# Optimization experiments

Hardware: AMD Instinct MI355X
Metric: run time of the kernel (lower is better)

Reference implementation:

```python
import jax, jax.numpy as jnp
import numpy as np

B, T, E_A, E_B, E_ATT, N_HEAD = 2, 2048, 2048, 2048, 2048, 16
HS = E_ATT // N_HEAD  # 128
ROPE_BASE = 100000.0


def setup_inputs() -> dict:
    key = jax.random.key(0)
    ks = jax.random.split(key, 6)
    Ta = T // 2
    x_a = jax.random.normal(ks[0], (B, Ta, E_A), jnp.float32)
    x_b = jax.random.normal(ks[1], (B, T - Ta, E_B), jnp.float32)
    # alternating text/other tokens: even positions are stream-a
    mask_a = jnp.tile((jnp.arange(T) % 2 == 0)[None, :], (B, 1))
    # standard RoPE tables, full head_size (freqs duplicated), as litgpt/nanoGPT build them
    pos = jnp.arange(T, dtype=jnp.float32)
    inv_freq = 1.0 / (ROPE_BASE ** (jnp.arange(0, HS, 2, dtype=jnp.float32) / HS))
    freqs = pos[:, None] * inv_freq[None, :]           # [T, HS/2]
    emb = jnp.concatenate([freqs, freqs], axis=-1)      # [T, HS]
    cos, sin = jnp.cos(emb), jnp.sin(emb)
    s = 0.02
    Wqkv_a = jax.random.normal(ks[2], (E_A, 3 * E_ATT), jnp.float32) * s
    Wqkv_b = jax.random.normal(ks[3], (E_B, 3 * E_ATT), jnp.float32) * s
    Wproj_a = jax.random.normal(ks[4], (E_ATT, E_A), jnp.float32) * s
    Wproj_b = jax.random.normal(ks[5], (E_ATT, E_B), jnp.float32) * s
    return dict(x_a=x_a, x_b=x_b, cos=cos, sin=sin, mask_a=mask_a,
                Wqkv_a=Wqkv_a, Wqkv_b=Wqkv_b, Wproj_a=Wproj_a, Wproj_b=Wproj_b)


def _apply_rope(x, cos, sin):
    # x: [B, H, T, HS]; cos/sin: [T, HS] broadcast over leading dims
    x1 = x[..., : HS // 2]
    x2 = x[..., HS // 2:]
    rot = jnp.concatenate([-x2, x1], axis=-1)
    return (x * cos + rot * sin).astype(x.dtype)


def reference(x_a, x_b, cos, sin, mask_a, Wqkv_a, Wqkv_b, Wproj_a, Wproj_b):
    Bm, Tm = mask_a.shape
    Na = x_a.shape[0] * x_a.shape[1]  # static token counts per stream
    Nb = x_b.shape[0] * x_b.shape[1]
    C3 = Wqkv_a.shape[1]              # 3 * E_ATT
    # dual-stream QKV projections (bias=False)
    qkv_a = (x_a @ Wqkv_a).reshape(-1, C3)
    qkv_b = (x_b @ Wqkv_b).reshape(-1, C3)
    # interleave tokens back into the full [B, T] layout by mask scatter
    flat = mask_a.reshape(-1)
    idx_a = jnp.nonzero(flat, size=Na)[0]
    idx_b = jnp.nonzero(~flat, size=Nb)[0]
    kqv = jnp.zeros((Bm * Tm, C3), qkv_a.dtype).at[idx_a].set(qkv_a).at[idx_b].set(qkv_b)
    kqv = kqv.reshape(Bm, Tm, 3 * N_HEAD, HS).transpose(0, 2, 1, 3)  # [B, 3H, T, hs]
    q, k, v = kqv[:, :N_HEAD], kqv[:, N_HEAD:2 * N_HEAD], kqv[:, 2 * N_HEAD:]
    q = _apply_rope(q, cos, sin)
    k = _apply_rope(k, cos, sin)
    # causal SDPA (dropout_p = 0 at eval)
    scale = 1.0 / np.sqrt(HS).astype(np.float32)
    att = jnp.einsum('bhqd,bhkd->bhqk', q, k) * scale
    causal = jnp.tril(jnp.ones((Tm, Tm), bool))
    att = jnp.where(causal, att, -jnp.inf)
    att = jax.nn.softmax(att, axis=-1)
    y = jnp.einsum('bhqk,bhkd->bhqd', att, v)
    y = y.transpose(0, 2, 1, 3).reshape(Bm * Tm, N_HEAD * HS)
    # mask split + per-stream output projections
    y_a = y[idx_a] @ Wproj_a
    y_b = y[idx_b] @ Wproj_b
    return (y_a, y_b)
```

## Files before the change

kernel.cpp:

```cpp
#include <hip/hip_runtime.h>
#include <hip/hip_bf16.h>


typedef __attribute__((ext_vector_type(8))) short v8s;
typedef __attribute__((ext_vector_type(4))) float v4f;

#define GL2LDS(gptr, lptr)                                              \
  __builtin_amdgcn_global_load_lds(                                     \
      (const __attribute__((address_space(1))) void*)(gptr),            \
      (__attribute__((address_space(3))) void*)(lptr), 16, 0, 0)

#define S_BARRIER() asm volatile("s_barrier" ::: "memory")

__device__ __forceinline__ float b2f(unsigned short u) {
  return __uint_as_float(((unsigned int)u) << 16);
}
__device__ __forceinline__ unsigned short f2bf(float f) {
  unsigned int u = __float_as_uint(f);
  u += 0x7fffu + ((u >> 16) & 1u);
  return (unsigned short)(u >> 16);
}

__global__ __launch_bounds__(256) void f32_to_bf16_2(
    const float4* __restrict__ a, const float4* __restrict__ b,
    uint2* __restrict__ out, int n4each) {
  int i = blockIdx.x * 256 + threadIdx.x;
  if (i >= 2 * n4each) return;
  float4 v = (i < n4each) ? a[i] : b[i - n4each];
  uint2 o;
  o.x = (unsigned int)f2bf(v.x) | ((unsigned int)f2bf(v.y) << 16);
  o.y = (unsigned int)f2bf(v.z) | ((unsigned int)f2bf(v.w) << 16);
  out[i] = o;
}

__global__ __launch_bounds__(256) void transpose_f32_bf16(
    const float* __restrict__ in0, const float* __restrict__ in1,
    unsigned short* __restrict__ out0, unsigned short* __restrict__ out1,
    int R, int C) {
  const float* in = blockIdx.z ? in1 : in0;
  unsigned short* out = blockIdx.z ? out1 : out0;
  __shared__ unsigned short tile[64][65];
  const int bc = blockIdx.x * 64, br = blockIdx.y * 64;
  const int c  = threadIdx.x & 63;
  const int r0 = threadIdx.x >> 6;
  for (int r = r0; r < 64; r += 4)
    tile[r][c] = f2bf(in[(size_t)(br + r) * C + bc + c]);
  __syncthreads();
  for (int rr = r0; rr < 64; rr += 4)
    out[(size_t)(bc + rr) * R + br + c] = tile[c][rr];
}

template <int MH, int NH>
__device__ __forceinline__ void mfma_quad(v4f (&acc)[8][4], const v8s (&a)[4][2],
                                          const v8s (&b)[4][2]) {
  __builtin_amdgcn_s_setprio(1);
#pragma unroll
  for (int ks = 0; ks < 2; ++ks)
#pragma unroll
    for (int i = 0; i < 4; ++i)
#pragma unroll
      for (int j = 0; j < 2; ++j)
        acc[MH * 4 + i][NH * 2 + j] = __builtin_amdgcn_mfma_f32_16x16x32_bf16(
            a[i][ks], b[NH * 2 + j][ks], acc[MH * 4 + i][NH * 2 + j], 0, 0, 0);
  __builtin_amdgcn_s_setprio(0);
}

__device__ __forceinline__ void read_a_half(const unsigned short* lds, int base,
                                            int mh, int r, int c0, int c1,
                                            v8s (&a)[4][2]) {
#pragma unroll
  for (int i = 0; i < 4; ++i) {
    const unsigned short* ap = lds + base + (mh * 64 + i * 16 + r) * 64;
    a[i][0] = *(const v8s*)(ap + c0);
    a[i][1] = *(const v8s*)(ap + c1);
  }
}

template <int NH>
__device__ __forceinline__ void read_b_half(const unsigned short* lds, int base,
                                            int brow, int r, int c0, int c1,
                                            v8s (&b)[4][2]) {
#pragma unroll
  for (int j = 0; j < 2; ++j) {
    const unsigned short* bp = lds + base + (brow + (NH * 2 + j) * 16 + r) * 64;
    b[NH * 2 + j][0] = *(const v8s*)(bp + c0);
    b[NH * 2 + j][1] = *(const v8s*)(bp + c1);
  }
}

template <int GATHER, int OSCAT>
__global__ __launch_bounds__(512, 2) void gemm256(
    const unsigned short* __restrict__ A,
    const unsigned short* __restrict__ BT0,
    const unsigned short* __restrict__ BT1,
    void* __restrict__ Cout, int M, int N, int K, int NBN) {
  __shared__ __align__(16) unsigned short lds[65536];
  const int tid = threadIdx.x;
  const int par = blockIdx.y;
  const unsigned short* __restrict__ BT = par ? BT1 : BT0;

  int wg = blockIdx.x;
  const int cpx = gridDim.x >> 3;
  wg = (wg & 7) * cpx + (wg >> 3);
  const int m0 = (wg / NBN) * 256, n0 = (wg % NBN) * 256;

  const int w = tid >> 6, lane = tid & 63;
  const int wm = w >> 2, wn = w & 3;
  const int r = lane & 15, q = lane >> 4;
  const int rs = r & 7;
  const int c0 = ((q ^ rs) << 3);
  const int c1 = (((4 + q) ^ rs) << 3);
  const int brow = (wn & 1) << 6;
  const int AbaseE = (2 + wm) * 8192, BbaseE = (wn >> 1) * 8192;
  const int AbaseO = (6 + wm) * 8192, BbaseO = (4 + (wn >> 1)) * 8192;

  const int sr0 = tid >> 3, sslot = tid & 7;
  const int NT = K >> 6, NIT = NT >> 1;

  auto stageB = [&](int p, int tt) {
    unsigned short* dst = &lds[(((tt << 2) + p) & 7) * 8192 + w * 512];
#pragma unroll
    for (int cc = 0; cc < 2; ++cc) {
      const int row = sr0 + cc * 64;
      const int g = ((sslot ^ (row & 7)) << 3);
      GL2LDS(BT + (size_t)(n0 + p * 128 + row) * K + tt * 64 + g, dst + cc * 4096);
    }
  };
  auto stageA = [&](int p, int tt) {
    unsigned short* dst = &lds[(((tt << 2) + 2 + p) & 7) * 8192 + w * 512];
#pragma unroll
    for (int cc = 0; cc < 2; ++cc) {
      const int row = sr0 + cc * 64;
      const int g = ((sslot ^ (row & 7)) << 3);
      int ar = m0 + p * 128 + row;
      if constexpr (GATHER) ar = ((ar >> 10) << 11) + ((ar & 1023) << 1) + par;
      GL2LDS(A + (size_t)ar * K + tt * 64 + g, dst + cc * 4096);
    }
  };

  v4f acc[8][4] = {};
  v8s a[4][2], b[4][2];

  stageB(0, 0); stageB(1, 0); stageA(0, 0); stageA(1, 0);
  asm volatile("" ::: "memory");
  stageB(0, 1); stageB(1, 1);
  asm volatile("s_waitcnt vmcnt(4)" ::: "memory");
  S_BARRIER();

  for (int it = 0; it < NIT; ++it) {
    const int t = it << 1;
    const bool more = (it + 1 < NIT);

    read_a_half(lds, AbaseE, 0, r, c0, c1, a);
    read_b_half<0>(lds, BbaseE, brow, r, c0, c1, b);
    stageA(0, t + 1);
    S_BARRIER();
    mfma_quad<0, 0>(acc, a, b);
    S_BARRIER();
    read_b_half<1>(lds, BbaseE, brow, r, c0, c1, b);
    stageA(1, t + 1);
    S_BARRIER();
    mfma_quad<0, 1>(acc, a, b);
    S_BARRIER();
    read_a_half(lds, AbaseE, 1, r, c0, c1, a);
    if (more) stageB(0, t + 2);
    S_BARRIER();
    mfma_quad<1, 0>(acc, a, b);
    S_BARRIER();
    if (more) stageB(1, t + 2);
    S_BARRIER();
    mfma_quad<1, 1>(acc, a, b);
    if (more) { asm volatile("s_waitcnt vmcnt(4)" ::: "memory"); }
    else      { asm volatile("s_waitcnt vmcnt(0)" ::: "memory"); }
    S_BARRIER();

    read_a_half(lds, AbaseO, 0, r, c0, c1, a);
    read_b_half<0>(lds, BbaseO, brow, r, c0, c1, b);
    if (more) stageA(0, t + 2);
    S_BARRIER();
    mfma_quad<0, 0>(acc, a, b);
    S_BARRIER();
    read_b_half<1>(lds, BbaseO, brow, r, c0, c1, b);
    if (more) stageA(1, t + 2);
    S_BARRIER();
    mfma_quad<0, 1>(acc, a, b);
    S_BARRIER();
    read_a_half(lds, AbaseO, 1, r, c0, c1, a);
    if (more) stageB(0, t + 3);
    S_BARRIER();
    mfma_quad<1, 0>(acc, a, b);
    S_BARRIER();
    if (more) stageB(1, t + 3);
    S_BARRIER();
    mfma_quad<1, 1>(acc, a, b);
    if (more) { asm volatile("s_waitcnt vmcnt(4)" ::: "memory"); }
    S_BARRIER();
  }

  float* Cf = (float*)Cout + (size_t)par * M * N;
  unsigned short* Cb = (unsigned short*)Cout;
#pragma unroll
  for (int tm = 0; tm < 8; ++tm) {
    const int rowm = m0 + wm * 128 + tm * 16 + q * 4;
#pragma unroll
    for (int tn = 0; tn < 4; ++tn) {
      const int col = n0 + wn * 64 + tn * 16 + r;
#pragma unroll
      for (int p = 0; p < 4; ++p) {
        if constexpr (OSCAT == 0) {
          Cf[(size_t)(rowm + p) * N + col] = acc[tm][tn][p];
        } else {
          const int ar = rowm + p;
          const int orow = ((ar >> 10) << 11) + ((ar & 1023) << 1) + (OSCAT - 1);
          Cb[(size_t)orow * N + col] = f2bf(acc[tm][tn][p]);
        }
      }
    }
  }
}

__global__ __launch_bounds__(256) void scatter_rope(
    const unsigned short* __restrict__ qkv,
    const float* __restrict__ cosb, const float* __restrict__ sinb,
    unsigned short* __restrict__ Q, unsigned short* __restrict__ K) {
  const int token = blockIdx.x;
  const int b = token >> 11, t = token & 2047;
  const unsigned short* src = qkv + (size_t)token * 6144;
  for (int i = threadIdx.x; i < 2048; i += 256) {
    const int d = i & 127, h = i >> 7;
    const float cv = cosb[t * 128 + d];
    const float sv = sinb[t * 128 + d];
    const int   mate = (d < 64) ? i + 64 : i - 64;
    const float sgn  = (d < 64) ? -1.f : 1.f;
    const float qv = b2f(src[i]),        qm = b2f(src[mate]) * sgn;
    const float kv = b2f(src[2048 + i]), km = b2f(src[2048 + mate]) * sgn;
    const size_t off = ((size_t)(b * 16 + h) * 2048 + t) * 128 + d;
    Q[off] = f2bf(qv * cv + qm * sv);
    K[off] = f2bf(kv * cv + km * sv);
  }
}

__global__ __launch_bounds__(256) void transpose_v(
    const unsigned short* __restrict__ qkv, unsigned short* __restrict__ Vt) {
  __shared__ unsigned short tile[128][129];
  const int bh = blockIdx.x >> 4, tt = blockIdx.x & 15;
  const int b = bh >> 4, h = bh & 15;
  const int tid = threadIdx.x;
  const int d0 = tid & 127, t0 = tid >> 7;
#pragma unroll 4
  for (int i = 0; i < 64; ++i) {
    int tl = i * 2 + t0;
    tile[tl][d0] =
        qkv[((size_t)(b * 2048 + tt * 128 + tl)) * 6144 + 4096 + h * 128 + d0];
  }
  __syncthreads();
#pragma unroll 4
  for (int i = 0; i < 64; ++i) {
    int dd = i * 2 + t0;
    Vt[((size_t)(bh * 128 + dd)) * 2048 + tt * 128 + d0] = tile[d0][dd];
  }
}

#define SIG 0.1275174038536989f

__global__ __launch_bounds__(256, 2) void attn_flash(
    const unsigned short* __restrict__ Q, const unsigned short* __restrict__ K,
    const unsigned short* __restrict__ Vt, unsigned short* __restrict__ Y) {
  __shared__ __align__(16) unsigned short Ks[2][64 * 128];
  __shared__ __align__(16) unsigned short Vs[2][128 * 64];
  __shared__ __align__(16) unsigned short Pl[64 * 72];

  const int x = blockIdx.x;
  const int bh = (x & 7) * 4 + ((x >> 3) & 3);
  const int pr = x >> 5;
  const int tid = threadIdx.x, w = tid >> 6, lane = tid & 63;
  const int r = lane & 15, q = lane >> 4;
  const int b = bh >> 4, h = bh & 15;
  const size_t kbase = (size_t)bh * 2048 * 128;
  const size_t vbase = (size_t)bh * 128 * 2048;
  const int vrow = lane >> 3, pc = lane & 7;

  for (int ph = 0; ph < 2; ++ph) {
    const int qt = ph ? pr : (31 - pr);

    const size_t qbase = ((size_t)bh * 2048 + qt * 64) * 128;
    v8s qf[4];
#pragma unroll
    for (int ki = 0; ki < 4; ++ki)
      qf[ki] = *(const v8s*)&Q[qbase + (size_t)(w * 16 + r) * 128 +
                               (ki * 4 + q) * 8];

    float mrun[4], lrun[4];
    v4f O[8] = {};
#pragma unroll
    for (int p = 0; p < 4; ++p) { mrun[p] = -3.0e38f; lrun[p] = 0.f; }

    const int nkt = qt + 1;

    auto stageKV = [&](int kt, int buf) {
#pragma unroll
      for (int i = 0; i < 4; ++i) {
        const int key = w * 16 + i * 4 + q;
        const int gs = r ^ (key & 15);
        GL2LDS(K + kbase + ((size_t)kt * 64 + key) * 128 + gs * 8,
               &Ks[buf][(w * 16 + i * 4) * 128]);
      }
#pragma unroll
      for (int i = 0; i < 4; ++i) {
        const int d = w * 32 + i * 8 + vrow;
        const int gs = pc ^ (d & 7);
        GL2LDS(Vt + vbase + (size_t)d * 2048 + kt * 64 + gs * 8,
               &Vs[buf][(w * 32 + i * 8) * 64]);
      }
    };

    stageKV(0, 0);
    for (int kt = 0; kt < nkt; ++kt) {
      const int buf = kt & 1;
      if (kt + 1 < nkt) {
        stageKV(kt + 1, buf ^ 1);
        asm volatile("s_waitcnt vmcnt(8)" ::: "memory");
      } else {
        asm volatile("s_waitcnt vmcnt(0)" ::: "memory");
      }
      S_BARRIER();

      v4f S[4] = {};
      __builtin_amdgcn_s_setprio(1);
#pragma unroll
      for (int ki = 0; ki < 4; ++ki) {
        v8s kf[4];
#pragma unroll
        for (int tn = 0; tn < 4; ++tn) {
          const int key = tn * 16 + r;
          const int c = (ki * 4 + q) ^ r;
          kf[tn] = *(const v8s*)&Ks[buf][key * 128 + c * 8];
        }
#pragma unroll
        for (int tn = 0; tn < 4; ++tn)
          S[tn] = __builtin_amdgcn_mfma_f32_16x16x32_bf16(
              qf[ki], kf[tn], S[tn], 0, 0, 0);
      }
      __builtin_amdgcn_s_setprio(0);

      if (kt == qt) {
#pragma unroll
        for (int tn = 0; tn < 4; ++tn)
#pragma unroll
          for (int p = 0; p < 4; ++p) {
            const int tq = w * 16 + q * 4 + p;
            const int kg = tn * 16 + r;
            if (kg > tq) S[tn][p] = -3.0e38f;
          }
      }

#pragma unroll
      for (int p = 0; p < 4; ++p) {
        float mx = fmaxf(fmaxf(S[0][p], S[1][p]), fmaxf(S[2][p], S[3][p]));
#pragma unroll
        for (int o = 1; o < 16; o <<= 1) mx = fmaxf(mx, __shfl_xor(mx, o, 64));
        const float mnew = fmaxf(mrun[p], mx);
        const float alpha = exp2f((mrun[p] - mnew) * SIG);
        mrun[p] = mnew;
        float sum = 0.f;
#pragma unroll
        for (int tn = 0; tn < 4; ++tn) {
          const float pv = exp2f((S[tn][p] - mnew) * SIG);
          S[tn][p] = pv;
          sum += pv;
        }
#pragma unroll
        for (int o = 1; o < 16; o <<= 1) sum += __shfl_xor(sum, o, 64);
        lrun[p] = lrun[p] * alpha + sum;
#pragma unroll
        for (int tn = 0; tn < 8; ++tn) O[tn][p] *= alpha;
      }

#pragma unroll
      for (int tn = 0; tn < 4; ++tn)
#pragma unroll
        for (int p = 0; p < 4; ++p) {
          const int m = w * 16 + q * 4 + p;
          Pl[m * 72 + tn * 16 + r] = f2bf(S[tn][p]);
        }

      __builtin_amdgcn_s_setprio(1);
#pragma unroll
      for (int ki = 0; ki < 2; ++ki) {
        v8s pf, vf[8];
        const int m = w * 16 + r;
        pf = *(const v8s*)&Pl[m * 72 + (ki * 4 + q) * 8];
#pragma unroll
        for (int tn = 0; tn < 8; ++tn) {
          const int d = tn * 16 + r;
          const int c = (ki * 4 + q) ^ (d & 7);
          vf[tn] = *(const v8s*)&Vs[buf][d * 64 + c * 8];
        }
#pragma unroll
        for (int tn = 0; tn < 8; ++tn)
          O[tn] = __builtin_amdgcn_mfma_f32_16x16x32_bf16(
              pf, vf[tn], O[tn], 0, 0, 0);
      }
      __builtin_amdgcn_s_setprio(0);

      asm volatile("s_waitcnt lgkmcnt(0)" ::: "memory");
      S_BARRIER();
    }

#pragma unroll
    for (int p = 0; p < 4; ++p) {
      const float inv = 1.0f / lrun[p];
      const int t = qt * 64 + w * 16 + q * 4 + p;
#pragma unroll
      for (int tn = 0; tn < 8; ++tn)
        Y[((size_t)(b * 2048 + t)) * 2048 + h * 128 + tn * 16 + r] =
            f2bf(O[tn][p] * inv);
    }
  }
}

extern "C" void kernel_launch(void* const* d_in, const int* in_sizes, int n_in,
                              void* d_out, int out_size, void* d_ws, size_t ws_size,
                              hipStream_t stream) {
  const float* x_a   = (const float*)d_in[0];
  const float* x_b   = (const float*)d_in[1];
  const float* cosb  = (const float*)d_in[2];
  const float* sinb  = (const float*)d_in[3];
  const float* Wqkv_a  = (const float*)d_in[5];
  const float* Wqkv_b  = (const float*)d_in[6];
  const float* Wproj_a = (const float*)d_in[7];
  const float* Wproj_b = (const float*)d_in[8];
  float* out = (float*)d_out;

  if (ws_size < 100663296u) return;

  char* ws = (char*)d_ws;
  unsigned short* QKVall = (unsigned short*)(ws);
  unsigned short* XA     = (unsigned short*)(ws + 50331648);
  unsigned short* WQT    = (unsigned short*)(ws + 67108864);
  unsigned short* Qb     = (unsigned short*)(ws + 50331648);
  unsigned short* Kb     = (unsigned short*)(ws + 67108864);
  unsigned short* Vtb    = (unsigned short*)(ws + 83886080);
  unsigned short* Yb     = (unsigned short*)(ws);
  unsigned short* WPT_A  = (unsigned short*)(ws + 16777216);
  unsigned short* WPT_B  = (unsigned short*)(ws + 25165824);

  hipLaunchKernelGGL(f32_to_bf16_2, dim3(8192), dim3(256), 0, stream,
                     (const float4*)x_a, (const float4*)x_b, (uint2*)XA, 1048576);
  hipLaunchKernelGGL(transpose_f32_bf16, dim3(96, 32, 1), dim3(256), 0, stream,
                     Wqkv_a, Wqkv_a, WQT, WQT, 2048, 6144);
  hipLaunchKernelGGL((gemm256<0, 1>), dim3(192, 1), dim3(512), 0, stream,
                     XA, WQT, WQT, QKVall, 2048, 6144, 2048, 24);
  hipLaunchKernelGGL(transpose_f32_bf16, dim3(96, 32, 1), dim3(256), 0, stream,
                     Wqkv_b, Wqkv_b, WQT, WQT, 2048, 6144);
  hipLaunchKernelGGL((gemm256<0, 2>), dim3(192, 1), dim3(512), 0, stream,
                     XA + (size_t)4194304, WQT, WQT, QKVall, 2048, 6144, 2048, 24);

  hipLaunchKernelGGL(scatter_rope, dim3(4096), dim3(256), 0, stream,
                     QKVall, cosb, sinb, Qb, Kb);
  hipLaunchKernelGGL(transpose_v, dim3(512), dim3(256), 0, stream,
                     QKVall, Vtb);

  hipLaunchKernelGGL(transpose_f32_bf16, dim3(32, 32, 2), dim3(256), 0, stream,
                     Wproj_a, Wproj_b, WPT_A, WPT_B, 2048, 2048);

  hipLaunchKernelGGL(attn_flash, dim3(512), dim3(256), 0, stream,
                     Qb, Kb, Vtb, Yb);

  hipLaunchKernelGGL((gemm256<1, 0>), dim3(64, 2), dim3(512), 0, stream,
                     Yb, WPT_A, WPT_B, out, 2048, 2048, 2048, 8);
}
```

Baseline: 495.9 us.

## Enlarge attention query tile to 128 rows with lazy softmax rescaling

The flash attention kernel now gives each wave 32 query rows (two 16-row groups) over a 128-row tile, so every K/V tile staged in shared memory feeds twice as many MFMAs. The grid is halved to 256 blocks with occupancy reduced to one block per CU. P staging moves to per-wave buffers, and the online softmax skips the running-max update and O rescale unless a row max grows past a threshold of 60 above the running max. This aims to cut LDS and global K/V traffic and rescale work per query. In exchange it raises register pressure, lowers occupancy and block count on a large-CU device, and risks fp32 overflow or precision loss from the deferred rescale.

```diff
diff --git a/kernel.cpp b/kernel.cpp
--- a/kernel.cpp
+++ b/kernel.cpp
@@ -263,12 +263,12 @@
 
 #define SIG 0.1275174038536989f
 
-__global__ __launch_bounds__(256, 2) void attn_flash(
+__global__ __launch_bounds__(256, 1) void attn_flash(
     const unsigned short* __restrict__ Q, const unsigned short* __restrict__ K,
     const unsigned short* __restrict__ Vt, unsigned short* __restrict__ Y) {
   __shared__ __align__(16) unsigned short Ks[2][64 * 128];
   __shared__ __align__(16) unsigned short Vs[2][128 * 64];
-  __shared__ __align__(16) unsigned short Pl[64 * 72];
+  __shared__ __align__(16) unsigned short Pl[4][32 * 72];
 
   const int x = blockIdx.x;
   const int bh = (x & 7) * 4 + ((x >> 3) & 3);
@@ -279,23 +279,29 @@
   const size_t kbase = (size_t)bh * 2048 * 128;
   const size_t vbase = (size_t)bh * 128 * 2048;
   const int vrow = lane >> 3, pc = lane & 7;
+  unsigned short* Pw = &Pl[w][0];
 
   for (int ph = 0; ph < 2; ++ph) {
-    const int qt = ph ? pr : (31 - pr);
-
-    const size_t qbase = ((size_t)bh * 2048 + qt * 64) * 128;
-    v8s qf[4];
-#pragma unroll
-    for (int ki = 0; ki < 4; ++ki)
-      qf[ki] = *(const v8s*)&Q[qbase + (size_t)(w * 16 + r) * 128 +
-                               (ki * 4 + q) * 8];
-
-    float mrun[4], lrun[4];
-    v4f O[8] = {};
-#pragma unroll
-    for (int p = 0; p < 4; ++p) { mrun[p] = -3.0e38f; lrun[p] = 0.f; }
-
-    const int nkt = qt + 1;
+    const int qt = ph ? pr : (15 - pr);
+
+    const size_t qbase = ((size_t)bh * 2048 + qt * 128) * 128;
+    v8s qf[2][4];
+#pragma unroll
+    for (int rg = 0; rg < 2; ++rg)
+#pragma unroll
+      for (int ki = 0; ki < 4; ++ki)
+        qf[rg][ki] = *(const v8s*)&Q[qbase +
+                                     (size_t)(w * 32 + rg * 16 + r) * 128 +
+                                     (ki * 4 + q) * 8];
+
+    float mrun[2][4], lrun[2][4];
+    v4f O[2][8] = {};
+#pragma unroll
+    for (int rg = 0; rg < 2; ++rg)
+#pragma unroll
+      for (int p = 0; p < 4; ++p) { mrun[rg][p] = -3.0e38f; lrun[rg][p] = 0.f; }
+
+    const int nkt = 2 * qt + 2;
 
     auto stageKV = [&](int kt, int buf) {
 #pragma unroll
@@ -325,7 +331,7 @@
       }
       S_BARRIER();
 
-      v4f S[4] = {};
+      v4f S[2][4] = {};
       __builtin_amdgcn_s_setprio(1);
 #pragma unroll
       for (int ki = 0; ki < 4; ++ki) {
@@ -337,69 +343,113 @@
           kf[tn] = *(const v8s*)&Ks[buf][key * 128 + c * 8];
         }
 #pragma unroll
+        for (int tn = 0; tn < 4; ++tn) {
+          S[0][tn] = __builtin_amdgcn_mfma_f32_16x16x32_bf16(
+              qf[0][ki], kf[tn], S[0][tn], 0, 0, 0);
+          S[1][tn] = __builtin_amdgcn_mfma_f32_16x16x32_bf16(
+              qf[1][ki], kf[tn], S[1][tn], 0, 0, 0);
+        }
+      }
+      __builtin_amdgcn_s_setprio(0);
+
+      if (kt >= nkt - 2) {
+        const int off = (kt - (nkt - 2)) * 64;
+#pragma unroll
+        for (int rg = 0; rg < 2; ++rg)
+#pragma unroll
+          for (int tn = 0; tn < 4; ++tn)
+#pragma unroll
+            for (int p = 0; p < 4; ++p) {
+              const int tq = w * 32 + rg * 16 + q * 4 + p;
+              const int kg = tn * 16 + r + off;
+              if (kg > tq) S[rg][tn][p] = -3.0e38f;
+            }
+      }
+
+      float mx[2][4];
+#pragma unroll
+      for (int rg = 0; rg < 2; ++rg)
+#pragma unroll
+        for (int p = 0; p < 4; ++p) {
+          float m0v = fmaxf(fmaxf(S[rg][0][p], S[rg][1][p]),
+                            fmaxf(S[rg][2][p], S[rg][3][p]));
+#pragma unroll
+          for (int o = 1; o < 16; o <<= 1) m0v = fmaxf(m0v, __shfl_xor(m0v, o, 64));
+          mx[rg][p] = m0v;
+        }
+      int need = 0;
+#pragma unroll
+      for (int rg = 0; rg < 2; ++rg)
+#pragma unroll
+        for (int p = 0; p < 4; ++p)
+          need |= (mx[rg][p] > mrun[rg][p] + 60.0f) ? 1 : 0;
+
+      if (__any(need)) {
+#pragma unroll
+        for (int rg = 0; rg < 2; ++rg)
+#pragma unroll
+          for (int p = 0; p < 4; ++p) {
+            const float mnew = fmaxf(mrun[rg][p], mx[rg][p]);
+            const float alpha = exp2f((mrun[rg][p] - mnew) * SIG);
+            mrun[rg][p] = mnew;
+            float sum = 0.f;
+#pragma unroll
+            for (int tn = 0; tn < 4; ++tn) {
+              const float pv = exp2f((S[rg][tn][p] - mnew) * SIG);
+              S[rg][tn][p] = pv;
+              sum += pv;
+            }
+#pragma unroll
+            for (int o = 1; o < 16; o <<= 1) sum += __shfl_xor(sum, o, 64);
+            lrun[rg][p] = lrun[rg][p] * alpha + sum;
+#pragma unroll
+            for (int tn = 0; tn < 8; ++tn) O[rg][tn][p] *= alpha;
+          }
+      } else {
+#pragma unroll
+        for (int rg = 0; rg < 2; ++rg)
+#pragma unroll
+          for (int p = 0; p < 4; ++p) {
+            float sum = 0.f;
+#pragma unroll
+            for (int tn = 0; tn < 4; ++tn) {
+              const float pv = exp2f((S[rg][tn][p] - mrun[rg][p]) * SIG);
+              S[rg][tn][p] = pv;
+              sum += pv;
+            }
+#pragma unroll
+            for (int o = 1; o < 16; o <<= 1) sum += __shfl_xor(sum, o, 64);
+            lrun[rg][p] += sum;
+          }
+      }
+
+#pragma unroll
+      for (int rg = 0; rg < 2; ++rg)
+#pragma unroll
         for (int tn = 0; tn < 4; ++tn)
-          S[tn] = __builtin_amdgcn_mfma_f32_16x16x32_bf16(
-              qf[ki], kf[tn], S[tn], 0, 0, 0);
-      }
-      __builtin_amdgcn_s_setprio(0);
-
-      if (kt == qt) {
-#pragma unroll
-        for (int tn = 0; tn < 4; ++tn)
-#pragma unroll
-          for (int p = 0; p < 4; ++p) {
-            const int tq = w * 16 + q * 4 + p;
-            const int kg = tn * 16 + r;
-            if (kg > tq) S[tn][p] = -3.0e38f;
-          }
-      }
-
-#pragma unroll
-      for (int p = 0; p < 4; ++p) {
-        float mx = fmaxf(fmaxf(S[0][p], S[1][p]), fmaxf(S[2][p], S[3][p]));
-#pragma unroll
-        for (int o = 1; o < 16; o <<= 1) mx = fmaxf(mx, __shfl_xor(mx, o, 64));
-        const float mnew = fmaxf(mrun[p], mx);
-        const float alpha = exp2f((mrun[p] - mnew) * SIG);
-        mrun[p] = mnew;
-        float sum = 0.f;
-#pragma unroll
-        for (int tn = 0; tn < 4; ++tn) {
-          const float pv = exp2f((S[tn][p] - mnew) * SIG);
-          S[tn][p] = pv;
-          sum += pv;
-        }
-#pragma unroll
-        for (int o = 1; o < 16; o <<= 1) sum += __shfl_xor(sum, o, 64);
-        lrun[p] = lrun[p] * alpha + sum;
-#pragma unroll
-        for (int tn = 0; tn < 8; ++tn) O[tn][p] *= alpha;
-      }
-
-#pragma unroll
-      for (int tn = 0; tn < 4; ++tn)
-#pragma unroll
-        for (int p = 0; p < 4; ++p) {
-          const int m = w * 16 + q * 4 + p;
-          Pl[m * 72 + tn * 16 + r] = f2bf(S[tn][p]);
-        }
+#pragma unroll
+          for (int p = 0; p < 4; ++p)
+            Pw[(rg * 16 + q * 4 + p) * 72 + tn * 16 + r] = f2bf(S[rg][tn][p]);
 
       __builtin_amdgcn_s_setprio(1);
 #pragma unroll
       for (int ki = 0; ki < 2; ++ki) {
-        v8s pf, vf[8];
-        const int m = w * 16 + r;
-        pf = *(const v8s*)&Pl[m * 72 + (ki * 4 + q) * 8];
+        v8s vf[8];
 #pragma unroll
         for (int tn = 0; tn < 8; ++tn) {
           const int d = tn * 16 + r;
           const int c = (ki * 4 + q) ^ (d & 7);
           vf[tn] = *(const v8s*)&Vs[buf][d * 64 + c * 8];
         }
-#pragma unroll
-        for (int tn = 0; tn < 8; ++tn)
-          O[tn] = __builtin_amdgcn_mfma_f32_16x16x32_bf16(
-              pf, vf[tn], O[tn], 0, 0, 0);
+        const v8s pf0 = *(const v8s*)&Pw[r * 72 + (ki * 4 + q) * 8];
+        const v8s pf1 = *(const v8s*)&Pw[(16 + r) * 72 + (ki * 4 + q) * 8];
+#pragma unroll
+        for (int tn = 0; tn < 8; ++tn) {
+          O[0][tn] = __builtin_amdgcn_mfma_f32_16x16x32_bf16(
+              pf0, vf[tn], O[0][tn], 0, 0, 0);
+          O[1][tn] = __builtin_amdgcn_mfma_f32_16x16x32_bf16(
+              pf1, vf[tn], O[1][tn], 0, 0, 0);
+        }
       }
       __builtin_amdgcn_s_setprio(0);
 
@@ -408,14 +458,16 @@
     }
 
 #pragma unroll
-    for (int p = 0; p < 4; ++p) {
-      const float inv = 1.0f / lrun[p];
-      const int t = qt * 64 + w * 16 + q * 4 + p;
-#pragma unroll
-      for (int tn = 0; tn < 8; ++tn)
-        Y[((size_t)(b * 2048 + t)) * 2048 + h * 128 + tn * 16 + r] =
-            f2bf(O[tn][p] * inv);
-    }
+    for (int rg = 0; rg < 2; ++rg)
+#pragma unroll
+      for (int p = 0; p < 4; ++p) {
+        const float inv = 1.0f / lrun[rg][p];
+        const int t = qt * 128 + w * 32 + rg * 16 + q * 4 + p;
+#pragma unroll
+        for (int tn = 0; tn < 8; ++tn)
+          Y[((size_t)(b * 2048 + t)) * 2048 + h * 128 + tn * 16 + r] =
+              f2bf(O[rg][tn][p] * inv);
+      }
   }
 }
 
@@ -464,7 +516,7 @@
   hipLaunchKernelGGL(transpose_f32_bf16, dim3(32, 32, 2), dim3(256), 0, stream,
                      Wproj_a, Wproj_b, WPT_A, WPT_B, 2048, 2048);
 
-  hipLaunchKernelGGL(attn_flash, dim3(512), dim3(256), 0, stream,
+  hipLaunchKernelGGL(attn_flash, dim3(256), dim3(256), 0, stream,
                      Qb, Kb, Vtb, Yb);
 
   hipLaunchKernelGGL((gemm256<1, 0>), dim3(64, 2), dim3(512), 0, stream,
```

Measured after the change: 536.9 us. 8.3% more time.
